# Optimization experiments

Hardware: AMD Instinct MI355X
Metric: run time of the kernel (lower is better)

## Reference

```python
import jax, jax.numpy as jnp
import numpy as np

NUM_NODES = 262144
NUM_GRAPHS = 256
D_MODEL = 256
LOG_2 = float(np.log(2.0))


def setup_inputs() -> dict:
    key = jax.random.key(0)
    k1, k2, k3 = jax.random.split(key, 3)
    l_enc = jax.random.normal(k1, (NUM_NODES, D_MODEL), dtype=jnp.float32)
    g_enc = jax.random.normal(k2, (NUM_GRAPHS, D_MODEL), dtype=jnp.float32)
    batch = jax.random.randint(k3, (NUM_NODES,), 0, NUM_GRAPHS, dtype=jnp.int64)
    return {"l_enc": l_enc, "g_enc": g_enc, "batch": batch}


def reference(l_enc, g_enc, batch):
    # local_global_loss_ with measure='JSD', mask=[] (msk == ones)
    num_nodes = l_enc.shape[0]
    num_graphs = g_enc.shape[0]
    # pos_mask: one-hot of graph id per node; neg_mask is its complement
    pos_mask = jax.nn.one_hot(batch, num_graphs, dtype=l_enc.dtype)  # [N, G]
    neg_mask = 1.0 - pos_mask
    res = jnp.einsum('nd,gd->ng', l_enc, g_enc)                      # [N, G]
    # JSD positive expectation on res*pos_mask (zeros contribute 0)
    Ep = LOG_2 - jax.nn.softplus(-(res * pos_mask))
    # JSD negative expectation on res*neg_mask (zeros contribute 0)
    rq = res * neg_mask
    Eq = jax.nn.softplus(-rq) + rq - LOG_2
    E_pos = jnp.sum(Ep) / num_nodes
    E_neg = jnp.sum(Eq) / (num_nodes * (num_graphs - 1))
    return E_neg - E_pos
```

## Files before the change

kernel.cpp:

```cpp
#include <hip/hip_runtime.h>
#include <hip/hip_bf16.h>

#define N_NODES 262144
#define N_GRAPHS 256
#define DMODEL 256
#define LN2 0.6931471805599453094

typedef __attribute__((ext_vector_type(4))) float f32x4;
typedef __attribute__((ext_vector_type(8))) short short8;

__device__ __forceinline__ short bf(float x) {
    __hip_bfloat16 h = __float2bfloat16(x);
    return __builtin_bit_cast(short, h);
}

__device__ __forceinline__ short8 cvt8(f32x4 lo, f32x4 hi) {
    short8 a;
    a[0] = bf(lo[0]); a[1] = bf(lo[1]); a[2] = bf(lo[2]); a[3] = bf(lo[3]);
    a[4] = bf(hi[0]); a[5] = bf(hi[1]); a[6] = bf(hi[2]); a[7] = bf(hi[3]);
    return a;
}

__device__ __forceinline__ void mfma8(short8 a, const char* bb, f32x4* acc) {
#pragma unroll
    for (int nt = 0; nt < 8; ++nt) {
        short8 bfrag = *reinterpret_cast<const short8*>(bb + nt * 1024);
        acc[nt] = __builtin_amdgcn_mfma_f32_16x16x32_bf16(a, bfrag, acc[nt], 0, 0, 0);
    }
}

__device__ __forceinline__ void elem(float r, int col, int bv,
                                     float& Sl2, float& Sl2p, float& Spr) {
    float t = fminf(r, 64.f) * 1.44269504f;
    float l2 = __log2f(1.f + exp2f(t));
    Sl2 += l2;
    float m = (col == bv) ? 1.f : 0.f;
    Sl2p = fmaf(m, l2, Sl2p);
    Spr = fmaf(m, r, Spr);
}

__global__ __launch_bounds__(512, 1) void mvgrl_main(
    const float* __restrict__ l_enc, const float* __restrict__ g_enc,
    const int* __restrict__ batch, double* __restrict__ partials) {
    extern __shared__ char lds_raw[];

    const int tid = threadIdx.x;
    const int lane = tid & 63;
    const int wave = tid >> 6;
    const int wrow = wave & 3;
    const int chalf = wave >> 2;

    const int row_blk = blockIdx.x * 1024;
    const int kofs = (lane >> 4) * 8;

    f32x4 A0l, A0h, A1l, A1h, A2l, A2h, A3l, A3h;
    f32x4 B0l, B0h, B1l, B1h, B2l, B2h, B3l, B3h;
    const float* arow0 = l_enc +
        (size_t)(row_blk + wrow * 16 + (lane & 15)) * DMODEL + kofs;
    A0l = *reinterpret_cast<const f32x4*>(arow0 + 0);
    A0h = *reinterpret_cast<const f32x4*>(arow0 + 4);
    A1l = *reinterpret_cast<const f32x4*>(arow0 + 32);
    A1h = *reinterpret_cast<const f32x4*>(arow0 + 36);
    A2l = *reinterpret_cast<const f32x4*>(arow0 + 64);
    A2h = *reinterpret_cast<const f32x4*>(arow0 + 68);
    A3l = *reinterpret_cast<const f32x4*>(arow0 + 96);
    A3h = *reinterpret_cast<const f32x4*>(arow0 + 100);
    B0l = *reinterpret_cast<const f32x4*>(arow0 + 128);
    B0h = *reinterpret_cast<const f32x4*>(arow0 + 132);
    B1l = *reinterpret_cast<const f32x4*>(arow0 + 160);
    B1h = *reinterpret_cast<const f32x4*>(arow0 + 164);
    B2l = *reinterpret_cast<const f32x4*>(arow0 + 192);
    B2h = *reinterpret_cast<const f32x4*>(arow0 + 196);
    B3l = *reinterpret_cast<const f32x4*>(arow0 + 224);
    B3h = *reinterpret_cast<const f32x4*>(arow0 + 228);

    {
        short8* lb = reinterpret_cast<short8*>(lds_raw);
#pragma unroll 2
        for (int i = 0; i < 16; ++i) {
            int c = wave + i * 8;
            int nt = c & 15, ks = c >> 4;
            int g = nt * 16 + (lane & 15);
            int k = ks * 32 + (lane >> 4) * 8;
            const float* src = g_enc + g * DMODEL + k;
            f32x4 lo = *reinterpret_cast<const f32x4*>(src);
            f32x4 hi = *reinterpret_cast<const f32x4*>(src + 4);
            lb[c * 64 + lane] = cvt8(lo, hi);
        }
    }
    __syncthreads();

    const char* ldsB = lds_raw + chalf * 8192 + lane * 16;
    double dS0 = 0.0, dS1 = 0.0, dS2 = 0.0;

#pragma unroll 1
    for (int pass = 0; pass < 16; ++pass) {
        const int rowbase = row_blk + pass * 64 + wrow * 16;
        const int rsub = (lane >> 4) * 4;
        int bv0 = batch[rowbase + rsub + 0];
        int bv1 = batch[rowbase + rsub + 1];
        int bv2 = batch[rowbase + rsub + 2];
        int bv3 = batch[rowbase + rsub + 3];

        const float* anext = l_enc +
            (size_t)(row_blk + ((pass + 1) & 15) * 64 + wrow * 16 + (lane & 15)) *
                DMODEL + kofs;

        f32x4 acc[8];
#pragma unroll
        for (int n = 0; n < 8; ++n) acc[n] = (f32x4){0.f, 0.f, 0.f, 0.f};

#pragma unroll 1
        for (int g = 0; g < 2; ++g) {
            if (g == 0) {
                {
                    short8 a = cvt8(A0l, A0h);
                    A0l = *reinterpret_cast<const f32x4*>(anext + 0);
                    A0h = *reinterpret_cast<const f32x4*>(anext + 4);
                    mfma8(a, ldsB + 0 * 16384, acc);
                }
                {
                    short8 a = cvt8(A1l, A1h);
                    A1l = *reinterpret_cast<const f32x4*>(anext + 32);
                    A1h = *reinterpret_cast<const f32x4*>(anext + 36);
                    mfma8(a, ldsB + 1 * 16384, acc);
                }
                {
                    short8 a = cvt8(A2l, A2h);
                    A2l = *reinterpret_cast<const f32x4*>(anext + 64);
                    A2h = *reinterpret_cast<const f32x4*>(anext + 68);
                    mfma8(a, ldsB + 2 * 16384, acc);
                }
                {
                    short8 a = cvt8(A3l, A3h);
                    A3l = *reinterpret_cast<const f32x4*>(anext + 96);
                    A3h = *reinterpret_cast<const f32x4*>(anext + 100);
                    mfma8(a, ldsB + 3 * 16384, acc);
                }
            } else {
                {
                    short8 a = cvt8(B0l, B0h);
                    B0l = *reinterpret_cast<const f32x4*>(anext + 128);
                    B0h = *reinterpret_cast<const f32x4*>(anext + 132);
                    mfma8(a, ldsB + 4 * 16384, acc);
                }
                {
                    short8 a = cvt8(B1l, B1h);
                    B1l = *reinterpret_cast<const f32x4*>(anext + 160);
                    B1h = *reinterpret_cast<const f32x4*>(anext + 164);
                    mfma8(a, ldsB + 5 * 16384, acc);
                }
                {
                    short8 a = cvt8(B2l, B2h);
                    B2l = *reinterpret_cast<const f32x4*>(anext + 192);
                    B2h = *reinterpret_cast<const f32x4*>(anext + 196);
                    mfma8(a, ldsB + 6 * 16384, acc);
                }
                {
                    short8 a = cvt8(B3l, B3h);
                    B3l = *reinterpret_cast<const f32x4*>(anext + 224);
                    B3h = *reinterpret_cast<const f32x4*>(anext + 228);
                    mfma8(a, ldsB + 7 * 16384, acc);
                }
            }
        }

        float Sl2 = 0.f, Sl2p = 0.f, Spr = 0.f;
        const int colbase = chalf * 128 + (lane & 15);
#pragma unroll
        for (int nt = 0; nt < 8; ++nt) {
            const int col = colbase + nt * 16;
            f32x4 av = acc[nt];
            elem(av[0], col, bv0, Sl2, Sl2p, Spr);
            elem(av[1], col, bv1, Sl2, Sl2p, Spr);
            elem(av[2], col, bv2, Sl2, Sl2p, Spr);
            elem(av[3], col, bv3, Sl2, Sl2p, Spr);
        }
        dS0 += (double)Sl2;
        dS1 += (double)Sl2p;
        dS2 += (double)Spr;
    }

#pragma unroll
    for (int off = 32; off; off >>= 1) {
        dS0 += __shfl_xor(dS0, off);
        dS1 += __shfl_xor(dS1, off);
        dS2 += __shfl_xor(dS2, off);
    }
    __syncthreads();
    double* red = reinterpret_cast<double*>(lds_raw);
    if (lane == 0) {
        red[wave * 3 + 0] = dS0;
        red[wave * 3 + 1] = dS1;
        red[wave * 3 + 2] = dS2;
    }
    __syncthreads();
    if (tid == 0) {
        double a = 0, b = 0, c = 0;
#pragma unroll
        for (int w = 0; w < 8; ++w) {
            a += red[w * 3 + 0];
            b += red[w * 3 + 1];
            c += red[w * 3 + 2];
        }
        partials[blockIdx.x * 3 + 0] = a;
        partials[blockIdx.x * 3 + 1] = b;
        partials[blockIdx.x * 3 + 2] = c;
    }
}

__global__ void finalize_kernel(const double* __restrict__ p,
                                float* __restrict__ out) {
    int t = threadIdx.x;
    double a = p[t * 3 + 0], b = p[t * 3 + 1], c = p[t * 3 + 2];
#pragma unroll
    for (int off = 32; off; off >>= 1) {
        a += __shfl_xor(a, off);
        b += __shfl_xor(b, off);
        c += __shfl_xor(c, off);
    }
    __shared__ double red[12];
    int lane = t & 63, w = t >> 6;
    if (lane == 0) { red[w * 3] = a; red[w * 3 + 1] = b; red[w * 3 + 2] = c; }
    __syncthreads();
    if (t == 0) {
        double A = 0, B = 0, C = 0;
#pragma unroll
        for (int i = 0; i < 4; ++i) {
            A += red[i * 3]; B += red[i * 3 + 1]; C += red[i * 3 + 2];
        }
        const double NN = (double)N_NODES, GG = (double)N_GRAPHS;
        double Sall_q = LN2 * A - NN * GG * LN2;
        double Spq = LN2 * B - NN * LN2;
        double Spr = C;
        double neg = (Sall_q - Spq) / (NN * (GG - 1.0));
        double pos = (Spr - Spq) / NN;
        out[0] = (float)(neg - pos);
    }
}

extern "C" void kernel_launch(void* const* d_in, const int* in_sizes, int n_in,
                              void* d_out, int out_size, void* d_ws,
                              size_t ws_size, hipStream_t stream) {
    const float* l_enc = (const float*)d_in[0];
    const float* g_enc = (const float*)d_in[1];
    const int* batch = (const int*)d_in[2];
    float* out = (float*)d_out;

    double* partials = (double*)d_ws;

    (void)hipFuncSetAttribute(reinterpret_cast<const void*>(mvgrl_main),
                              hipFuncAttributeMaxDynamicSharedMemorySize, 131072);

    mvgrl_main<<<256, 512, 131072, stream>>>(l_enc, g_enc, batch, partials);
    finalize_kernel<<<1, 256, 0, stream>>>(partials, out);
}
```

Baseline: 91.59 us.

## Split column halves across blocks and halve A prefetch registers

Each block now covers one half of the graph columns, using 4 waves and 64KB of LDS, and 512 blocks run instead of 256. The bid mapping places the two column halves of the same row group in nearby blocks so the shared l_enc rows can be reused from L2. The A-operand prefetch now uses a single 8-register set, reloaded with the second K half and then the next pass's first half, which lowers register pressure. The trade-off is that each l_enc tile is read twice, once per column half, which doubles global and L2 traffic for A. In exchange, more blocks can be resident and the grid fills more CUs.

```diff
diff --git a/kernel.cpp b/kernel.cpp
--- a/kernel.cpp
+++ b/kernel.cpp
@@ -39,7 +39,7 @@
     Spr = fmaf(m, r, Spr);
 }
 
-__global__ __launch_bounds__(512, 1) void mvgrl_main(
+__global__ __launch_bounds__(256, 1) void mvgrl_main(
     const float* __restrict__ l_enc, const float* __restrict__ g_enc,
     const int* __restrict__ batch, double* __restrict__ partials) {
     extern __shared__ char lds_raw[];
@@ -47,40 +47,32 @@
     const int tid = threadIdx.x;
     const int lane = tid & 63;
     const int wave = tid >> 6;
-    const int wrow = wave & 3;
-    const int chalf = wave >> 2;
-
-    const int row_blk = blockIdx.x * 1024;
+    const int bid = blockIdx.x;
+
+    const int rg = (bid >> 4) * 8 + (bid & 7);
+    const int chalf = (bid >> 3) & 1;
+    const int row_blk = rg * 1024;
     const int kofs = (lane >> 4) * 8;
 
-    f32x4 A0l, A0h, A1l, A1h, A2l, A2h, A3l, A3h;
-    f32x4 B0l, B0h, B1l, B1h, B2l, B2h, B3l, B3h;
-    const float* arow0 = l_enc +
-        (size_t)(row_blk + wrow * 16 + (lane & 15)) * DMODEL + kofs;
-    A0l = *reinterpret_cast<const f32x4*>(arow0 + 0);
-    A0h = *reinterpret_cast<const f32x4*>(arow0 + 4);
-    A1l = *reinterpret_cast<const f32x4*>(arow0 + 32);
-    A1h = *reinterpret_cast<const f32x4*>(arow0 + 36);
-    A2l = *reinterpret_cast<const f32x4*>(arow0 + 64);
-    A2h = *reinterpret_cast<const f32x4*>(arow0 + 68);
-    A3l = *reinterpret_cast<const f32x4*>(arow0 + 96);
-    A3h = *reinterpret_cast<const f32x4*>(arow0 + 100);
-    B0l = *reinterpret_cast<const f32x4*>(arow0 + 128);
-    B0h = *reinterpret_cast<const f32x4*>(arow0 + 132);
-    B1l = *reinterpret_cast<const f32x4*>(arow0 + 160);
-    B1h = *reinterpret_cast<const f32x4*>(arow0 + 164);
-    B2l = *reinterpret_cast<const f32x4*>(arow0 + 192);
-    B2h = *reinterpret_cast<const f32x4*>(arow0 + 196);
-    B3l = *reinterpret_cast<const f32x4*>(arow0 + 224);
-    B3h = *reinterpret_cast<const f32x4*>(arow0 + 228);
+    f32x4 s0l, s0h, s1l, s1h, s2l, s2h, s3l, s3h;
+    const float* arow = l_enc +
+        (size_t)(row_blk + wave * 16 + (lane & 15)) * DMODEL + kofs;
+    s0l = *reinterpret_cast<const f32x4*>(arow + 0);
+    s0h = *reinterpret_cast<const f32x4*>(arow + 4);
+    s1l = *reinterpret_cast<const f32x4*>(arow + 32);
+    s1h = *reinterpret_cast<const f32x4*>(arow + 36);
+    s2l = *reinterpret_cast<const f32x4*>(arow + 64);
+    s2h = *reinterpret_cast<const f32x4*>(arow + 68);
+    s3l = *reinterpret_cast<const f32x4*>(arow + 96);
+    s3h = *reinterpret_cast<const f32x4*>(arow + 100);
 
     {
         short8* lb = reinterpret_cast<short8*>(lds_raw);
 #pragma unroll 2
         for (int i = 0; i < 16; ++i) {
-            int c = wave + i * 8;
-            int nt = c & 15, ks = c >> 4;
-            int g = nt * 16 + (lane & 15);
+            int c = wave + i * 4;
+            int nt = c & 7, ks = c >> 3;
+            int g = chalf * 128 + nt * 16 + (lane & 15);
             int k = ks * 32 + (lane >> 4) * 8;
             const float* src = g_enc + g * DMODEL + k;
             f32x4 lo = *reinterpret_cast<const f32x4*>(src);
@@ -90,20 +82,20 @@
     }
     __syncthreads();
 
-    const char* ldsB = lds_raw + chalf * 8192 + lane * 16;
+    const char* ldsB = lds_raw + lane * 16;
     double dS0 = 0.0, dS1 = 0.0, dS2 = 0.0;
 
 #pragma unroll 1
     for (int pass = 0; pass < 16; ++pass) {
-        const int rowbase = row_blk + pass * 64 + wrow * 16;
+        const int rowbase = row_blk + pass * 64 + wave * 16;
         const int rsub = (lane >> 4) * 4;
         int bv0 = batch[rowbase + rsub + 0];
         int bv1 = batch[rowbase + rsub + 1];
         int bv2 = batch[rowbase + rsub + 2];
         int bv3 = batch[rowbase + rsub + 3];
 
-        const float* anext = l_enc +
-            (size_t)(row_blk + ((pass + 1) & 15) * 64 + wrow * 16 + (lane & 15)) *
+        const float* arow_next = l_enc +
+            (size_t)(row_blk + ((pass + 1) & 15) * 64 + wave * 16 + (lane & 15)) *
                 DMODEL + kofs;
 
         f32x4 acc[8];
@@ -112,58 +104,34 @@
 
 #pragma unroll 1
         for (int g = 0; g < 2; ++g) {
-            if (g == 0) {
-                {
-                    short8 a = cvt8(A0l, A0h);
-                    A0l = *reinterpret_cast<const f32x4*>(anext + 0);
-                    A0h = *reinterpret_cast<const f32x4*>(anext + 4);
-                    mfma8(a, ldsB + 0 * 16384, acc);
-                }
-                {
-                    short8 a = cvt8(A1l, A1h);
-                    A1l = *reinterpret_cast<const f32x4*>(anext + 32);
-                    A1h = *reinterpret_cast<const f32x4*>(anext + 36);
-                    mfma8(a, ldsB + 1 * 16384, acc);
-                }
-                {
-                    short8 a = cvt8(A2l, A2h);
-                    A2l = *reinterpret_cast<const f32x4*>(anext + 64);
-                    A2h = *reinterpret_cast<const f32x4*>(anext + 68);
-                    mfma8(a, ldsB + 2 * 16384, acc);
-                }
-                {
-                    short8 a = cvt8(A3l, A3h);
-                    A3l = *reinterpret_cast<const f32x4*>(anext + 96);
-                    A3h = *reinterpret_cast<const f32x4*>(anext + 100);
-                    mfma8(a, ldsB + 3 * 16384, acc);
-                }
-            } else {
-                {
-                    short8 a = cvt8(B0l, B0h);
-                    B0l = *reinterpret_cast<const f32x4*>(anext + 128);
-                    B0h = *reinterpret_cast<const f32x4*>(anext + 132);
-                    mfma8(a, ldsB + 4 * 16384, acc);
-                }
-                {
-                    short8 a = cvt8(B1l, B1h);
-                    B1l = *reinterpret_cast<const f32x4*>(anext + 160);
-                    B1h = *reinterpret_cast<const f32x4*>(anext + 164);
-                    mfma8(a, ldsB + 5 * 16384, acc);
-                }
-                {
-                    short8 a = cvt8(B2l, B2h);
-                    B2l = *reinterpret_cast<const f32x4*>(anext + 192);
-                    B2h = *reinterpret_cast<const f32x4*>(anext + 196);
-                    mfma8(a, ldsB + 6 * 16384, acc);
-                }
-                {
-                    short8 a = cvt8(B3l, B3h);
-                    B3l = *reinterpret_cast<const f32x4*>(anext + 224);
-                    B3h = *reinterpret_cast<const f32x4*>(anext + 228);
-                    mfma8(a, ldsB + 7 * 16384, acc);
-                }
-            }
-        }
+            const float* src = (g == 0) ? (arow + 128) : arow_next;
+            const char* lb = ldsB + (size_t)g * 4 * 8192;
+            {
+                short8 a = cvt8(s0l, s0h);
+                s0l = *reinterpret_cast<const f32x4*>(src + 0);
+                s0h = *reinterpret_cast<const f32x4*>(src + 4);
+                mfma8(a, lb + 0 * 8192, acc);
+            }
+            {
+                short8 a = cvt8(s1l, s1h);
+                s1l = *reinterpret_cast<const f32x4*>(src + 32);
+                s1h = *reinterpret_cast<const f32x4*>(src + 36);
+                mfma8(a, lb + 1 * 8192, acc);
+            }
+            {
+                short8 a = cvt8(s2l, s2h);
+                s2l = *reinterpret_cast<const f32x4*>(src + 64);
+                s2h = *reinterpret_cast<const f32x4*>(src + 68);
+                mfma8(a, lb + 2 * 8192, acc);
+            }
+            {
+                short8 a = cvt8(s3l, s3h);
+                s3l = *reinterpret_cast<const f32x4*>(src + 96);
+                s3h = *reinterpret_cast<const f32x4*>(src + 100);
+                mfma8(a, lb + 3 * 8192, acc);
+            }
+        }
+        arow = arow_next;
 
         float Sl2 = 0.f, Sl2p = 0.f, Spr = 0.f;
         const int colbase = chalf * 128 + (lane & 15);
@@ -198,14 +166,14 @@
     if (tid == 0) {
         double a = 0, b = 0, c = 0;
 #pragma unroll
-        for (int w = 0; w < 8; ++w) {
+        for (int w = 0; w < 4; ++w) {
             a += red[w * 3 + 0];
             b += red[w * 3 + 1];
             c += red[w * 3 + 2];
         }
-        partials[blockIdx.x * 3 + 0] = a;
-        partials[blockIdx.x * 3 + 1] = b;
-        partials[blockIdx.x * 3 + 2] = c;
+        partials[bid * 3 + 0] = a;
+        partials[bid * 3 + 1] = b;
+        partials[bid * 3 + 2] = c;
     }
 }
 
@@ -219,14 +187,14 @@
         b += __shfl_xor(b, off);
         c += __shfl_xor(c, off);
     }
-    __shared__ double red[12];
+    __shared__ double red[24];
     int lane = t & 63, w = t >> 6;
     if (lane == 0) { red[w * 3] = a; red[w * 3 + 1] = b; red[w * 3 + 2] = c; }
     __syncthreads();
     if (t == 0) {
         double A = 0, B = 0, C = 0;
 #pragma unroll
-        for (int i = 0; i < 4; ++i) {
+        for (int i = 0; i < 8; ++i) {
             A += red[i * 3]; B += red[i * 3 + 1]; C += red[i * 3 + 2];
         }
         const double NN = (double)N_NODES, GG = (double)N_GRAPHS;
@@ -250,8 +218,8 @@
     double* partials = (double*)d_ws;
 
     (void)hipFuncSetAttribute(reinterpret_cast<const void*>(mvgrl_main),
-                              hipFuncAttributeMaxDynamicSharedMemorySize, 131072);
-
-    mvgrl_main<<<256, 512, 131072, stream>>>(l_enc, g_enc, batch, partials);
-    finalize_kernel<<<1, 256, 0, stream>>>(partials, out);
-}
+                              hipFuncAttributeMaxDynamicSharedMemorySize, 65536);
+
+    mvgrl_main<<<512, 256, 65536, stream>>>(l_enc, g_enc, batch, partials);
+    finalize_kernel<<<1, 512, 0, stream>>>(partials, out);
+}
```

Measured after the change: 83.86 us. 8.4% less time.
